# Optimization experiments

Measured on AMD Instinct MI355X. Metric: run time of the kernel, lower is better.

The kernel has to match this reference:

```python
import jax, jax.numpy as jnp
import numpy as np

D_MODEL = 256
D_INNER = 512
D_STATE = 16
DT_RANK = 16
D_CONV = 4


def _layernorm(x, g, b):
    m = x.mean(-1, keepdims=True)
    v = jnp.mean((x - m) ** 2, axis=-1, keepdims=True)
    return (x - m) * jax.lax.rsqrt(v + 1e-5) * g + b


def _mamba(x, p):
    # x: (B, L, D); faithful to mamba_ssm Mamba forward (selective_scan_ref)
    in_w, conv_w, conv_b, xp_w, dt_w, dt_b, A_log, Dp, out_w = p
    B, L, _ = x.shape
    xz = x @ in_w.T                                   # (B, L, 2*d_inner)
    xi, z = jnp.split(xz, 2, axis=-1)
    # causal depthwise conv over time (d_conv=4), truncated to L
    xpad = jnp.pad(xi, ((0, 0), (D_CONV - 1, 0), (0, 0)))
    xc = conv_b + sum(xpad[:, k:k + L, :] * conv_w[:, k] for k in range(D_CONV))
    xc = jax.nn.silu(xc)                              # u: (B, L, d_inner)
    dbl = xc @ xp_w.T                                 # (B, L, dt_rank + 2*d_state)
    dt = dbl[..., :DT_RANK]
    Bm = dbl[..., DT_RANK:DT_RANK + D_STATE]          # (B, L, n)
    Cm = dbl[..., DT_RANK + D_STATE:]                 # (B, L, n)
    delta = jax.nn.softplus(dt @ dt_w.T + dt_b)       # (B, L, d_inner)
    A = -jnp.exp(A_log)                               # (d_inner, n)
    dA = jnp.exp(jnp.einsum('bld,dn->bldn', delta, A))
    dBu = jnp.einsum('bld,bln,bld->bldn', delta, Bm, xc)

    def step(h, inp):
        dA_t, dBu_t, C_t = inp
        h = dA_t * h + dBu_t                          # (B, d_inner, n)
        return h, jnp.einsum('bdn,bn->bd', h, C_t)

    h0 = jnp.zeros((B, D_INNER, D_STATE), x.dtype)
    _, ys = jax.lax.scan(step, h0, (dA.transpose(1, 0, 2, 3),
                                    dBu.transpose(1, 0, 2, 3),
                                    Cm.transpose(1, 0, 2)))
    y = ys.transpose(1, 0, 2) + xc * Dp               # (B, L, d_inner)
    y = y * jax.nn.silu(z)
    return y @ out_w.T                                # (B, L, D)


def _encoder(layer_params, x):
    # layer_params leaves have leading axis = num_layers (3)
    def step(carry, p):
        h = _layernorm(carry, p[0], p[1])
        return h + _mamba(h, p[2:]), None
    out, _ = jax.lax.scan(step, x, layer_params)
    return out


def _forward(x1, x2, x3, x4, audio, vis_w, vis_b, ln_g, ln_b, in_w, conv_w,
             conv_b, xp_w, dt_w, dt_b, A_log, Dp, out_w, gate_w, gate_b):
    gamma = 1.0
    bt = x1.shape[0]
    B = bt // 10
    d = x1.shape[1]
    pooled = [x.mean((2, 3)).reshape(B, 10, d) for x in (x1, x2, x3, x4)]
    vis = [p @ vis_w[i].T + vis_b[i] for i, p in enumerate(pooled)]
    # encoders 0..3: audio, 4..7: video scales
    stacked = jnp.stack([audio, audio, audio, audio] + vis)     # (8, B, 10, d)
    enc_params = (ln_g, ln_b, in_w, conv_w, conv_b, xp_w, dt_w, dt_b, A_log, Dp, out_w)
    outs = jax.vmap(_encoder)(enc_params, stacked)              # (8, B, 10, d)
    gates = jax.nn.silu(jnp.einsum('ebld,eod->eblo', outs, gate_w)
                        + gate_b[:, None, None, :])
    # NOTE: gate1 is reshaped WITHOUT transpose (faithful to original code)
    ag1 = gates[0].reshape(bt, d, 1, 1)
    ag2 = jnp.transpose(gates[1], (1, 0, 2)).reshape(bt, d, 1, 1)
    ag3 = jnp.transpose(gates[2], (1, 0, 2)).reshape(bt, d, 1, 1)
    ag4 = jnp.transpose(gates[3], (1, 0, 2)).reshape(bt, d, 1, 1)
    vg = sum(jnp.transpose(gates[4 + i], (1, 0, 2)).reshape(bt, d)
             for i in range(4)) / 4.0
    x1o = x1 + ag1 * x1 * gamma
    x2o = x2 + ag2 * x2 * gamma
    x3o = x3 + ag3 * x3 * gamma
    x4o = x4 + ag4 * x4 * gamma
    af = audio.reshape(bt, d)
    ao = (af + vg * af * gamma)[:, :, None]                     # (bt, d, 1)
    return (x4o, x3o, x2o, x1o, ao)


def setup_inputs() -> dict:
    key = jax.random.key(0)
    ks = jax.random.split(key, 24)
    s = 0.05
    n = lambda k, shp: jax.random.normal(k, shp, dtype=jnp.float32)
    inp = {
        'x1': n(ks[0], (40, 256, 56, 56)),
        'x2': n(ks[1], (40, 256, 28, 28)),
        'x3': n(ks[2], (40, 256, 14, 14)),
        'x4': n(ks[3], (40, 256, 7, 7)),
        'audio': n(ks[4], (4, 10, 256)),
        'vis_w': n(ks[5], (4, 256, 256)) * s,
        'vis_b': n(ks[6], (4, 256)) * s,
        'ln_g': jnp.ones((8, 3, 256), jnp.float32),
        'ln_b': jnp.zeros((8, 3, 256), jnp.float32),
        'in_w': n(ks[7], (8, 3, 1024, 256)) * s,
        'conv_w': n(ks[8], (8, 3, 512, 4)) * s,
        'conv_b': n(ks[9], (8, 3, 512)) * s,
        'xp_w': n(ks[10], (8, 3, 48, 512)) * s,
        'dt_w': n(ks[11], (8, 3, 512, 16)) * s,
        'dt_b': n(ks[12], (8, 3, 512)) * s,
        'A_log': jnp.broadcast_to(jnp.log(jnp.arange(1, 17, dtype=jnp.float32)),
                                  (8, 3, 512, 16)) + 0.0,
        'Dp': jnp.ones((8, 3, 512), jnp.float32),
        'out_w': n(ks[13], (8, 3, 256, 512)) * s,
        'gate_w': n(ks[14], (8, 256, 256)) * s,
        'gate_b': n(ks[15], (8, 256)) * s,
    }
    return inp


def reference(x1, x2, x3, x4, audio, vis_w, vis_b, ln_g, ln_b, in_w, conv_w,
              conv_b, xp_w, dt_w, dt_b, A_log, Dp, out_w, gate_w, gate_b):
    return _forward(x1, x2, x3, x4, audio, vis_w, vis_b, ln_g, ln_b, in_w,
                    conv_w, conv_b, xp_w, dt_w, dt_b, A_log, Dp, out_w,
                    gate_w, gate_b)
```

## Files before the change

### kernel.cpp

```cpp
#include <hip/hip_runtime.h>

#define DM 256
#define DI 512
#define NL 10

#define WS_POOLED 0
#define WS_GATES  40960
#define WS_SX     122880
#define WS_SH     204800
#define WS_XC     286720
#define WS_SZ     450560
#define WS_Y2     614400

__device__ __forceinline__ float dot4(float4 a, float4 b) {
    return a.x*b.x + a.y*b.y + a.z*b.z + a.w*b.w;
}
__device__ __forceinline__ float silu(float x) {
    return x / (1.f + __expf(-x));
}

__global__ void pool_kernel(const float* __restrict__ x1, const float* __restrict__ x2,
                            const float* __restrict__ x3, const float* __restrict__ x4,
                            const float* __restrict__ audio, float* __restrict__ ws)
{
    if (blockIdx.x >= 10240) {
        const int idx = blockIdx.x - 10240, e = idx >> 2, b = idx & 3;
        float* sx = ws + WS_SX + (e*4+b)*2560;
        for (int i = threadIdx.x; i < 2560; i += 256) sx[i] = audio[b*2560 + i];
        return;
    }
    float* pooled = ws + WS_POOLED;
    int wid  = (blockIdx.x * blockDim.x + threadIdx.x) >> 6;
    int lane = threadIdx.x & 63;
    int img = wid / 10240;
    int r   = wid % 10240;
    const float* src; int hw;
    if      (img == 0) { src = x1; hw = 3136; }
    else if (img == 1) { src = x2; hw = 784; }
    else if (img == 2) { src = x3; hw = 196; }
    else               { src = x4; hw = 49; }
    const float* row = src + (size_t)r * hw;
    float s = 0.f;
    if (hw == 49) {
        if (lane < 49) s = row[lane];
    } else {
        int n4 = hw >> 2;
        for (int j = lane; j < n4; j += 64) {
            float4 v = *(const float4*)(row + j*4);
            s += v.x + v.y + v.z + v.w;
        }
    }
    #pragma unroll
    for (int off = 32; off; off >>= 1) s += __shfl_down(s, off);
    if (lane == 0) pooled[img*10240 + r] = s / (float)hw;
}

__global__ __launch_bounds__(256)
void build_kernel(const float* __restrict__ vis_w, const float* __restrict__ vis_b,
                  float* __restrict__ ws)
{
    __shared__ float act[NL*DM];
    const int tid = threadIdx.x, bi = blockIdx.x;
    const int img = bi >> 6, b = (bi >> 4) & 3, tile = bi & 15;
    const float* pooled = ws + WS_POOLED + img*10240 + b*2560;
    for (int i = tid; i < 640; i += 256)
        ((float4*)act)[i] = ((const float4*)pooled)[i];
    __syncthreads();
    const int wave = tid >> 6, lane = tid & 63;
    const int c4 = lane >> 4, k16 = lane & 15;
    const int col = tile*16 + wave*4 + c4;
    const float* wp = vis_w + img*65536 + col*256 + k16*4;
    float acc[NL];
    #pragma unroll
    for (int l = 0; l < NL; l++) acc[l] = 0.f;
    #pragma unroll
    for (int ko = 0; ko < 4; ko++) {
        float4 wv = *(const float4*)(wp + ko*64);
        #pragma unroll
        for (int l = 0; l < NL; l++)
            acc[l] += dot4(wv, *(const float4*)(&act[l*256 + ko*64 + k16*4]));
    }
    #pragma unroll
    for (int l = 0; l < NL; l++) {
        acc[l] += __shfl_xor(acc[l], 1);
        acc[l] += __shfl_xor(acc[l], 2);
        acc[l] += __shfl_xor(acc[l], 4);
        acc[l] += __shfl_xor(acc[l], 8);
    }
    if (k16 == 0) {
        float bias = vis_b[img*256 + col];
        float* sx = ws + WS_SX + ((img+4)*4+b)*2560;
        #pragma unroll
        for (int l = 0; l < NL; l++) sx[l*256 + col] = bias + acc[l];
    }
}

__global__ __launch_bounds__(256)
void lnxz_kernel(const float* __restrict__ ln_g, const float* __restrict__ ln_b,
                 const float* __restrict__ in_w, const float* __restrict__ conv_w,
                 const float* __restrict__ conv_b, float* __restrict__ ws, int layer)
{
    __shared__ float act[NL*DM];
    const int tid = threadIdx.x, bi = blockIdx.x;
    const int e = bi >> 8, b = (bi >> 6) & 3, tile = bi & 63;
    const int el = e*3 + layer;
    const int wave = tid >> 6, lane = tid & 63;
    const float* sx = ws + WS_SX + (e*4+b)*2560;
    float* shg = ws + WS_SH + (e*4+b)*2560;

    for (int l = wave; l < NL; l += 4) {
        float4 v = *(const float4*)(sx + l*256 + lane*4);
        float s = v.x+v.y+v.z+v.w, ss = dot4(v, v);
        #pragma unroll
        for (int off = 32; off; off >>= 1) { s += __shfl_xor(s, off); ss += __shfl_xor(ss, off); }
        float m = s * (1.f/256.f);
        float rs = rsqrtf(ss*(1.f/256.f) - m*m + 1e-5f);
        float4 gv = *(const float4*)(ln_g + el*256 + lane*4);
        float4 bv = *(const float4*)(ln_b + el*256 + lane*4);
        float4 hv;
        hv.x = (v.x-m)*rs*gv.x + bv.x;
        hv.y = (v.y-m)*rs*gv.y + bv.y;
        hv.z = (v.z-m)*rs*gv.z + bv.z;
        hv.w = (v.w-m)*rs*gv.w + bv.w;
        *(float4*)(&act[l*256 + lane*4]) = hv;
        if (tile == 0) *(float4*)(shg + l*256 + lane*4) = hv;
    }
    __syncthreads();

    const int c4 = lane >> 4, k16 = lane & 15;
    const int col = tile*16 + wave*4 + c4;
    const float* wp = in_w + (size_t)el*262144 + (size_t)col*256 + k16*4;
    float acc[NL];
    #pragma unroll
    for (int l = 0; l < NL; l++) acc[l] = 0.f;
    #pragma unroll
    for (int ko = 0; ko < 4; ko++) {
        float4 wv = *(const float4*)(wp + ko*64);
        #pragma unroll
        for (int l = 0; l < NL; l++)
            acc[l] += dot4(wv, *(const float4*)(&act[l*256 + ko*64 + k16*4]));
    }
    #pragma unroll
    for (int l = 0; l < NL; l++) {
        acc[l] += __shfl_xor(acc[l], 1);
        acc[l] += __shfl_xor(acc[l], 2);
        acc[l] += __shfl_xor(acc[l], 4);
        acc[l] += __shfl_xor(acc[l], 8);
    }
    if (k16 == 0) {
        if (col < 512) {
            float4 cw = *(const float4*)(conv_w + el*2048 + col*4);
            float cb = conv_b[el*512 + col];
            float* xc = ws + WS_XC + (e*4+b)*5120;
            float x0 = 0.f, x1 = 0.f, x2 = 0.f;
            #pragma unroll
            for (int l = 0; l < NL; l++) {
                float x3 = acc[l];
                float a = cb + x3*cw.w + x2*cw.z + x1*cw.y + x0*cw.x;
                xc[l*512 + col] = silu(a);
                x0 = x1; x1 = x2; x2 = x3;
            }
        } else {
            float* sz = ws + WS_SZ + (e*4+b)*5120;
            const int d = col - 512;
            #pragma unroll
            for (int l = 0; l < NL; l++) sz[l*512 + d] = silu(acc[l]);
        }
    }
}

__global__ __launch_bounds__(256)
void dblscan2_kernel(const float* __restrict__ xp_w, const float* __restrict__ dt_w,
                     const float* __restrict__ dt_b, const float* __restrict__ A_log,
                     const float* __restrict__ Dp,   float* __restrict__ ws, int layer)
{
    __shared__ float xc_l[NL*DI];
    __shared__ float dbl_l[NL*48];
    const int tid = threadIdx.x, bi = blockIdx.x;
    const int e = bi >> 4, b = (bi >> 2) & 3, ch = bi & 3;
    const int el = e*3 + layer, eb = e*4 + b;
    const float* xc = ws + WS_XC + eb*5120;

    for (int i = tid; i < 1280; i += 256)
        ((float4*)xc_l)[i] = ((const float4*)xc)[i];
    __syncthreads();

    {
        const int wave = tid >> 6, lane = tid & 63;
        const int c4 = lane >> 4, k16 = lane & 15;
        for (int i = 0; i < 30; i++) {
            int t = wave*120 + i*4 + c4;
            int l = t / 48, r = t % 48;
            const float* wp = xp_w + el*24576 + r*512 + k16*4;
            float p = 0.f;
            #pragma unroll
            for (int ko = 0; ko < 8; ko++)
                p += dot4(*(const float4*)(wp + ko*64),
                          *(const float4*)(&xc_l[l*512 + ko*64 + k16*4]));
            p += __shfl_xor(p, 1);
            p += __shfl_xor(p, 2);
            p += __shfl_xor(p, 4);
            p += __shfl_xor(p, 8);
            if (k16 == 0) dbl_l[l*48 + r] = p;
        }
    }
    __syncthreads();

    {
        const int d = ch*128 + (tid >> 1);
        const int half = tid & 1;
        const float* dwp = dt_w + el*8192 + d*16;
        float4 dw0 = *(const float4*)(dwp);
        float4 dw1 = *(const float4*)(dwp + 4);
        float4 dw2 = *(const float4*)(dwp + 8);
        float4 dw3 = *(const float4*)(dwp + 12);
        float dbv = dt_b[el*512 + d];
        float Dpv = Dp[el*512 + d];
        float Av[8];
        #pragma unroll
        for (int j = 0; j < 8; j++)
            Av[j] = -__expf(A_log[el*8192 + d*16 + half*8 + j]);
        const float* sz = ws + WS_SZ + eb*5120;
        float* y2 = ws + WS_Y2 + eb*5120;
        float h[8];
        #pragma unroll
        for (int j = 0; j < 8; j++) h[j] = 0.f;
        #pragma unroll
        for (int l = 0; l < NL; l++) {
            float4 t0 = *(const float4*)(&dbl_l[l*48]);
            float4 t1 = *(const float4*)(&dbl_l[l*48 + 4]);
            float4 t2 = *(const float4*)(&dbl_l[l*48 + 8]);
            float4 t3 = *(const float4*)(&dbl_l[l*48 + 12]);
            float a = dbv + dot4(t0,dw0) + dot4(t1,dw1) + dot4(t2,dw2) + dot4(t3,dw3);
            float dl = fmaxf(a, 0.f) + log1pf(__expf(-fabsf(a)));
            float xcv = xc_l[l*512 + d];
            float du = dl * xcv;
            float y = 0.f;
            #pragma unroll
            for (int j = 0; j < 8; j++) {
                float Bn = dbl_l[l*48 + 16 + half*8 + j];
                float Cn = dbl_l[l*48 + 32 + half*8 + j];
                h[j] = __expf(dl*Av[j])*h[j] + du*Bn;
                y += h[j]*Cn;
            }
            y += __shfl_xor(y, 1);
            if (!half) y2[l*512 + d] = (y + xcv*Dpv) * sz[l*512 + d];
        }
    }
}

__global__ __launch_bounds__(256)
void out_kernel(const float* __restrict__ out_w, float* __restrict__ ws, int layer)
{
    __shared__ float act[NL*DI];
    const int tid = threadIdx.x, bi = blockIdx.x;
    const int e = bi >> 6, b = (bi >> 4) & 3, tile = bi & 15;
    const int el = e*3 + layer;
    const float* y2 = ws + WS_Y2 + (e*4+b)*5120;
    for (int i = tid; i < 1280; i += 256)
        ((float4*)act)[i] = ((const float4*)y2)[i];
    __syncthreads();

    const int wave = tid >> 6, lane = tid & 63;
    const int c4 = lane >> 4, k16 = lane & 15;
    const int col = tile*16 + wave*4 + c4;
    const float* wp = out_w + (size_t)el*131072 + (size_t)col*512 + k16*4;
    float acc[NL];
    #pragma unroll
    for (int l = 0; l < NL; l++) acc[l] = 0.f;
    #pragma unroll
    for (int ko = 0; ko < 8; ko++) {
        float4 wv = *(const float4*)(wp + ko*64);
        #pragma unroll
        for (int l = 0; l < NL; l++)
            acc[l] += dot4(wv, *(const float4*)(&act[l*512 + ko*64 + k16*4]));
    }
    #pragma unroll
    for (int l = 0; l < NL; l++) {
        acc[l] += __shfl_xor(acc[l], 1);
        acc[l] += __shfl_xor(acc[l], 2);
        acc[l] += __shfl_xor(acc[l], 4);
        acc[l] += __shfl_xor(acc[l], 8);
    }
    if (k16 == 0) {
        const float* sh = ws + WS_SH + (e*4+b)*2560;
        float* sx = ws + WS_SX + (e*4+b)*2560;
        #pragma unroll
        for (int l = 0; l < NL; l++) sx[l*256 + col] = sh[l*256 + col] + acc[l];
    }
}

__global__ __launch_bounds__(256)
void gate_kernel(const float* __restrict__ gate_w, const float* __restrict__ gate_b,
                 float* __restrict__ ws)
{
    __shared__ float act[NL*DM];
    const int tid = threadIdx.x, bi = blockIdx.x;
    const int e = bi >> 6, b = (bi >> 4) & 3, tile = bi & 15;
    const float* sx = ws + WS_SX + (e*4+b)*2560;
    for (int i = tid; i < 640; i += 256)
        ((float4*)act)[i] = ((const float4*)sx)[i];
    __syncthreads();

    const int wave = tid >> 6, lane = tid & 63;
    const int c4 = lane >> 4, k16 = lane & 15;
    const int col = tile*16 + wave*4 + c4;
    const float* wp = gate_w + e*65536 + col*256 + k16*4;
    float acc[NL];
    #pragma unroll
    for (int l = 0; l < NL; l++) acc[l] = 0.f;
    #pragma unroll
    for (int ko = 0; ko < 4; ko++) {
        float4 wv = *(const float4*)(wp + ko*64);
        #pragma unroll
        for (int l = 0; l < NL; l++)
            acc[l] += dot4(wv, *(const float4*)(&act[l*256 + ko*64 + k16*4]));
    }
    #pragma unroll
    for (int l = 0; l < NL; l++) {
        acc[l] += __shfl_xor(acc[l], 1);
        acc[l] += __shfl_xor(acc[l], 2);
        acc[l] += __shfl_xor(acc[l], 4);
        acc[l] += __shfl_xor(acc[l], 8);
    }
    if (k16 == 0) {
        float gb = gate_b[e*256 + col];
        float* gates = ws + WS_GATES;
        #pragma unroll
        for (int l = 0; l < NL; l++)
            gates[(e*40 + b*10 + l)*256 + col] = silu(gb + acc[l]);
    }
}

__global__ void scale_ao_kernel(const float* __restrict__ x1, const float* __restrict__ x2,
                                const float* __restrict__ x3, const float* __restrict__ x4,
                                const float* __restrict__ audio,
                                const float* __restrict__ gates, float* __restrict__ out)
{
    int wid  = (blockIdx.x * blockDim.x + threadIdx.x) >> 6;
    int lane = threadIdx.x & 63;
    if (wid >= 41120) return;
    if (wid >= 40960) {
        int i = (wid - 40960)*64 + lane;
        int bt = i >> 8, c = i & 255;
        int lb = (bt & 3)*10 + (bt >> 2);
        float vg = 0.25f * (gates[(160 + lb)*256 + c] + gates[(200 + lb)*256 + c] +
                            gates[(240 + lb)*256 + c] + gates[(280 + lb)*256 + c]);
        out[42649600 + i] = audio[i] * (1.f + vg);
        return;
    }
    int t = wid / 10240, r = wid % 10240;
    int bt = r >> 8, c = r & 255;
    int lb = (bt & 3)*10 + (bt >> 2);
    const float* src; int hw; size_t obase; int gidx;
    if      (t == 0) { src = x4; hw = 49;   obase = 0;        gidx = (120 + lb)*256 + c; }
    else if (t == 1) { src = x3; hw = 196;  obase = 501760;   gidx = ( 80 + lb)*256 + c; }
    else if (t == 2) { src = x2; hw = 784;  obase = 2508800;  gidx = ( 40 + lb)*256 + c; }
    else             { src = x1; hw = 3136; obase = 10536960; gidx = r; }
    float scale = 1.f + gates[gidx];
    const float* row = src + (size_t)r * hw;
    float* orow = out + obase + (size_t)r * hw;
    if (hw == 49) {
        if (lane < 49) orow[lane] = row[lane] * scale;
    } else {
        int n4 = hw >> 2;
        for (int j = lane; j < n4; j += 64) {
            float4 v = *(const float4*)(row + j*4);
            v.x *= scale; v.y *= scale; v.z *= scale; v.w *= scale;
            *(float4*)(orow + j*4) = v;
        }
    }
}

extern "C" void kernel_launch(void* const* d_in, const int* in_sizes, int n_in,
                              void* d_out, int out_size, void* d_ws, size_t ws_size,
                              hipStream_t stream)
{
    const float* x1     = (const float*)d_in[0];
    const float* x2     = (const float*)d_in[1];
    const float* x3     = (const float*)d_in[2];
    const float* x4     = (const float*)d_in[3];
    const float* audio  = (const float*)d_in[4];
    const float* vis_w  = (const float*)d_in[5];
    const float* vis_b  = (const float*)d_in[6];
    const float* ln_g   = (const float*)d_in[7];
    const float* ln_b   = (const float*)d_in[8];
    const float* in_w   = (const float*)d_in[9];
    const float* conv_w = (const float*)d_in[10];
    const float* conv_b = (const float*)d_in[11];
    const float* xp_w   = (const float*)d_in[12];
    const float* dt_w   = (const float*)d_in[13];
    const float* dt_b   = (const float*)d_in[14];
    const float* A_log  = (const float*)d_in[15];
    const float* Dp     = (const float*)d_in[16];
    const float* out_w  = (const float*)d_in[17];
    const float* gate_w = (const float*)d_in[18];
    const float* gate_b = (const float*)d_in[19];

    float* ws  = (float*)d_ws;
    float* out = (float*)d_out;

    pool_kernel<<<dim3(10256), dim3(256), 0, stream>>>(x1, x2, x3, x4, audio, ws);
    build_kernel<<<dim3(256), dim3(256), 0, stream>>>(vis_w, vis_b, ws);
    for (int layer = 0; layer < 3; layer++) {
        lnxz_kernel<<<dim3(2048), dim3(256), 0, stream>>>(ln_g, ln_b, in_w, conv_w,
                                                          conv_b, ws, layer);
        dblscan2_kernel<<<dim3(128), dim3(256), 0, stream>>>(xp_w, dt_w, dt_b, A_log,
                                                             Dp, ws, layer);
        out_kernel<<<dim3(512), dim3(256), 0, stream>>>(out_w, ws, layer);
    }
    gate_kernel<<<dim3(512), dim3(256), 0, stream>>>(gate_w, gate_b, ws);
    scale_ao_kernel<<<dim3(10280), dim3(256), 0, stream>>>(x1, x2, x3, x4, audio,
                                                           ws + WS_GATES, out);
}
```

Before: 247.7 us.

## Fuse gate GEMV into scale kernel and split scan across more blocks

Removes the separate gate kernel by having each wave of the final scaling kernel compute its own gate value with a 256-wide dot product and wave reduction before scaling its row. The audio path now spends one wave per output element to average four expert gates. Separately, the scan kernel is split into 256 blocks with four lanes per channel instead of two, which raises parallelism. In exchange, the xp_w projection is recomputed by twice as many blocks, and the fused kernel launches more waves that do redundant weight reads.

```diff
diff --git a/kernel.cpp b/kernel.cpp
--- a/kernel.cpp
+++ b/kernel.cpp
@@ -5,7 +5,6 @@
 #define NL 10
 
 #define WS_POOLED 0
-#define WS_GATES  40960
 #define WS_SX     122880
 #define WS_SH     204800
 #define WS_XC     286720
@@ -170,15 +169,16 @@
 }
 
 __global__ __launch_bounds__(256)
-void dblscan2_kernel(const float* __restrict__ xp_w, const float* __restrict__ dt_w,
-                     const float* __restrict__ dt_b, const float* __restrict__ A_log,
-                     const float* __restrict__ Dp,   float* __restrict__ ws, int layer)
+void dso2_kernel(const float* __restrict__ xp_w, const float* __restrict__ dt_w,
+                 const float* __restrict__ dt_b, const float* __restrict__ A_log,
+                 const float* __restrict__ Dp,   float* __restrict__ ws, int layer)
 {
     __shared__ float xc_l[NL*DI];
     __shared__ float dbl_l[NL*48];
     const int tid = threadIdx.x, bi = blockIdx.x;
-    const int e = bi >> 4, b = (bi >> 2) & 3, ch = bi & 3;
-    const int el = e*3 + layer, eb = e*4 + b;
+    const int eb = bi >> 3, slice = bi & 7;
+    const int e = eb >> 2;
+    const int el = e*3 + layer;
     const float* xc = ws + WS_XC + eb*5120;
 
     for (int i = tid; i < 1280; i += 256)
@@ -207,8 +207,8 @@
     __syncthreads();
 
     {
-        const int d = ch*128 + (tid >> 1);
-        const int half = tid & 1;
+        const int d = slice*64 + (tid >> 2);
+        const int q = tid & 3;
         const float* dwp = dt_w + el*8192 + d*16;
         float4 dw0 = *(const float4*)(dwp);
         float4 dw1 = *(const float4*)(dwp + 4);
@@ -216,15 +216,15 @@
         float4 dw3 = *(const float4*)(dwp + 12);
         float dbv = dt_b[el*512 + d];
         float Dpv = Dp[el*512 + d];
-        float Av[8];
-        #pragma unroll
-        for (int j = 0; j < 8; j++)
-            Av[j] = -__expf(A_log[el*8192 + d*16 + half*8 + j]);
+        float Av[4];
+        #pragma unroll
+        for (int j = 0; j < 4; j++)
+            Av[j] = -__expf(A_log[el*8192 + d*16 + q*4 + j]);
         const float* sz = ws + WS_SZ + eb*5120;
         float* y2 = ws + WS_Y2 + eb*5120;
-        float h[8];
-        #pragma unroll
-        for (int j = 0; j < 8; j++) h[j] = 0.f;
+        float h[4];
+        #pragma unroll
+        for (int j = 0; j < 4; j++) h[j] = 0.f;
         #pragma unroll
         for (int l = 0; l < NL; l++) {
             float4 t0 = *(const float4*)(&dbl_l[l*48]);
@@ -237,14 +237,15 @@
             float du = dl * xcv;
             float y = 0.f;
             #pragma unroll
-            for (int j = 0; j < 8; j++) {
-                float Bn = dbl_l[l*48 + 16 + half*8 + j];
-                float Cn = dbl_l[l*48 + 32 + half*8 + j];
+            for (int j = 0; j < 4; j++) {
+                float Bn = dbl_l[l*48 + 16 + q*4 + j];
+                float Cn = dbl_l[l*48 + 32 + q*4 + j];
                 h[j] = __expf(dl*Av[j])*h[j] + du*Bn;
                 y += h[j]*Cn;
             }
             y += __shfl_xor(y, 1);
-            if (!half) y2[l*512 + d] = (y + xcv*Dpv) * sz[l*512 + d];
+            y += __shfl_xor(y, 2);
+            if (q == 0) y2[l*512 + d] = (y + xcv*Dpv) * sz[l*512 + d];
         }
     }
 }
@@ -290,74 +291,57 @@
     }
 }
 
-__global__ __launch_bounds__(256)
-void gate_kernel(const float* __restrict__ gate_w, const float* __restrict__ gate_b,
-                 float* __restrict__ ws)
-{
-    __shared__ float act[NL*DM];
-    const int tid = threadIdx.x, bi = blockIdx.x;
-    const int e = bi >> 6, b = (bi >> 4) & 3, tile = bi & 15;
-    const float* sx = ws + WS_SX + (e*4+b)*2560;
-    for (int i = tid; i < 640; i += 256)
-        ((float4*)act)[i] = ((const float4*)sx)[i];
-    __syncthreads();
-
-    const int wave = tid >> 6, lane = tid & 63;
-    const int c4 = lane >> 4, k16 = lane & 15;
-    const int col = tile*16 + wave*4 + c4;
-    const float* wp = gate_w + e*65536 + col*256 + k16*4;
-    float acc[NL];
-    #pragma unroll
-    for (int l = 0; l < NL; l++) acc[l] = 0.f;
-    #pragma unroll
-    for (int ko = 0; ko < 4; ko++) {
-        float4 wv = *(const float4*)(wp + ko*64);
-        #pragma unroll
-        for (int l = 0; l < NL; l++)
-            acc[l] += dot4(wv, *(const float4*)(&act[l*256 + ko*64 + k16*4]));
-    }
-    #pragma unroll
-    for (int l = 0; l < NL; l++) {
-        acc[l] += __shfl_xor(acc[l], 1);
-        acc[l] += __shfl_xor(acc[l], 2);
-        acc[l] += __shfl_xor(acc[l], 4);
-        acc[l] += __shfl_xor(acc[l], 8);
-    }
-    if (k16 == 0) {
-        float gb = gate_b[e*256 + col];
-        float* gates = ws + WS_GATES;
-        #pragma unroll
-        for (int l = 0; l < NL; l++)
-            gates[(e*40 + b*10 + l)*256 + col] = silu(gb + acc[l]);
-    }
-}
-
-__global__ void scale_ao_kernel(const float* __restrict__ x1, const float* __restrict__ x2,
-                                const float* __restrict__ x3, const float* __restrict__ x4,
-                                const float* __restrict__ audio,
-                                const float* __restrict__ gates, float* __restrict__ out)
+__global__ void scale_ao_gate_kernel(const float* __restrict__ x1, const float* __restrict__ x2,
+                                     const float* __restrict__ x3, const float* __restrict__ x4,
+                                     const float* __restrict__ audio,
+                                     const float* __restrict__ gate_w,
+                                     const float* __restrict__ gate_b,
+                                     const float* __restrict__ ws, float* __restrict__ out)
 {
     int wid  = (blockIdx.x * blockDim.x + threadIdx.x) >> 6;
     int lane = threadIdx.x & 63;
-    if (wid >= 41120) return;
+    const float* sxB = ws + WS_SX;
+    if (wid >= 51200) return;
     if (wid >= 40960) {
-        int i = (wid - 40960)*64 + lane;
+        int i = wid - 40960;
         int bt = i >> 8, c = i & 255;
-        int lb = (bt & 3)*10 + (bt >> 2);
-        float vg = 0.25f * (gates[(160 + lb)*256 + c] + gates[(200 + lb)*256 + c] +
-                            gates[(240 + lb)*256 + c] + gates[(280 + lb)*256 + c]);
-        out[42649600 + i] = audio[i] * (1.f + vg);
+        int b = bt & 3, l = bt >> 2;
+        int c4 = lane >> 4, k16 = lane & 15;
+        int e = 4 + c4;
+        const float* gw = gate_w + e*65536 + c*256;
+        const float* sxrow = sxB + (e*4+b)*2560 + l*256;
+        float p = 0.f;
+        #pragma unroll
+        for (int ko = 0; ko < 4; ko++)
+            p += dot4(*(const float4*)(gw + ko*64 + k16*4),
+                      *(const float4*)(sxrow + ko*64 + k16*4));
+        p += __shfl_xor(p, 1);
+        p += __shfl_xor(p, 2);
+        p += __shfl_xor(p, 4);
+        p += __shfl_xor(p, 8);
+        float g = silu(gate_b[e*256 + c] + p);
+        g += __shfl_xor(g, 16);
+        g += __shfl_xor(g, 32);
+        if (lane == 0) out[42649600 + i] = audio[bt*256 + c] * (1.f + 0.25f*g);
         return;
     }
     int t = wid / 10240, r = wid % 10240;
     int bt = r >> 8, c = r & 255;
-    int lb = (bt & 3)*10 + (bt >> 2);
-    const float* src; int hw; size_t obase; int gidx;
-    if      (t == 0) { src = x4; hw = 49;   obase = 0;        gidx = (120 + lb)*256 + c; }
-    else if (t == 1) { src = x3; hw = 196;  obase = 501760;   gidx = ( 80 + lb)*256 + c; }
-    else if (t == 2) { src = x2; hw = 784;  obase = 2508800;  gidx = ( 40 + lb)*256 + c; }
-    else             { src = x1; hw = 3136; obase = 10536960; gidx = r; }
-    float scale = 1.f + gates[gidx];
+    int e, b, l;
+    if (t == 3) { e = 0; b = bt / 10; l = bt % 10; }
+    else        { e = 3 - t; b = bt & 3; l = bt >> 2; }
+    const float* gw = gate_w + e*65536 + c*256;
+    const float* sxrow = sxB + (e*4+b)*2560 + l*256;
+    float p = dot4(*(const float4*)(gw + lane*4), *(const float4*)(sxrow + lane*4));
+    #pragma unroll
+    for (int off = 32; off; off >>= 1) p += __shfl_xor(p, off);
+    float scale = 1.f + silu(gate_b[e*256 + c] + p);
+
+    const float* src; int hw; size_t obase;
+    if      (t == 0) { src = x4; hw = 49;   obase = 0; }
+    else if (t == 1) { src = x3; hw = 196;  obase = 501760; }
+    else if (t == 2) { src = x2; hw = 784;  obase = 2508800; }
+    else             { src = x1; hw = 3136; obase = 10536960; }
     const float* row = src + (size_t)r * hw;
     float* orow = out + obase + (size_t)r * hw;
     if (hw == 49) {
@@ -405,11 +389,10 @@
     for (int layer = 0; layer < 3; layer++) {
         lnxz_kernel<<<dim3(2048), dim3(256), 0, stream>>>(ln_g, ln_b, in_w, conv_w,
                                                           conv_b, ws, layer);
-        dblscan2_kernel<<<dim3(128), dim3(256), 0, stream>>>(xp_w, dt_w, dt_b, A_log,
-                                                             Dp, ws, layer);
+        dso2_kernel<<<dim3(256), dim3(256), 0, stream>>>(xp_w, dt_w, dt_b, A_log,
+                                                         Dp, ws, layer);
         out_kernel<<<dim3(512), dim3(256), 0, stream>>>(out_w, ws, layer);
     }
-    gate_kernel<<<dim3(512), dim3(256), 0, stream>>>(gate_w, gate_b, ws);
-    scale_ao_kernel<<<dim3(10280), dim3(256), 0, stream>>>(x1, x2, x3, x4, audio,
-                                                           ws + WS_GATES, out);
-}
+    scale_ao_gate_kernel<<<dim3(12800), dim3(256), 0, stream>>>(x1, x2, x3, x4, audio,
+                                                                gate_w, gate_b, ws, out);
+}
```

Measured after the change: 260.4 us. 1.05x slower.
